# Performance work log

Measured on AMD Instinct MI355X. Metric: run time of the kernel, lower is better.

The kernel has to match this reference:

```python
import jax, jax.numpy as jnp
import numpy as np

N_NODES = 100000
N_EDGES = 1600000
D_IN = 128
D_OUT = 128


def setup_inputs() -> dict:
    key = jax.random.key(0)
    k_x, k_r, k_c, k_v, k_w = jax.random.split(key, 5)
    X = jax.random.normal(k_x, (N_NODES, D_IN), dtype=jnp.float32)
    A_rows = jax.random.randint(k_r, (N_EDGES,), 0, N_NODES, dtype=jnp.int32)
    A_cols = jax.random.randint(k_c, (N_EDGES,), 0, N_NODES, dtype=jnp.int32)
    A_vals = jax.random.uniform(k_v, (N_EDGES,), dtype=jnp.float32)
    # Xavier-uniform linear weight [out, in], zero bias (matches reset_parameters)
    limit = float(np.sqrt(6.0 / (D_IN + D_OUT)))
    W = jax.random.uniform(k_w, (D_OUT, D_IN), dtype=jnp.float32, minval=-limit, maxval=limit)
    b = jnp.zeros((D_OUT,), dtype=jnp.float32)
    return {"X": X, "A_rows": A_rows, "A_cols": A_cols, "A_vals": A_vals, "W": W, "b": b}


def reference(X, A_rows, A_cols, A_vals, W, b):
    # h = A_sparse @ X  (COO SpMM: gather neighbor features, scale, scatter-add by row)
    msgs = A_vals[:, None] * X[A_cols]          # [E, D_IN]
    h = jax.ops.segment_sum(msgs, A_rows, num_segments=N_NODES)  # [N, D_IN]
    # dense linear projection
    return h @ W.T + b
```

## Files before the change

kernel.cpp:

```cpp
#include <hip/hip_runtime.h>

#define N_NODES_C 100000
#define N_EDGES_C 1600000
#define D_C 128
#define NBKT 1563
#define RPB 64
#define CAP 1536
#define PTILE 4096
#define NPB ((N_EDGES_C + PTILE - 1) / PTILE)
#define NGB ((N_NODES_C + 63) / 64)
#define WB_STRIDE 136

static __device__ __forceinline__ unsigned short f2bf(float x) {
    unsigned u = __float_as_uint(x);
    unsigned r = 0x7fffu + ((u >> 16) & 1u);
    return (unsigned short)((u + r) >> 16);
}
static __device__ __forceinline__ float bflo(unsigned u) { return __uint_as_float(u << 16); }
static __device__ __forceinline__ float bfhi(unsigned u) { return __uint_as_float(u & 0xffff0000u); }

typedef __attribute__((ext_vector_type(8))) __bf16 bf16x8;
typedef __attribute__((ext_vector_type(4))) float f32x4;
union FragU { uint4 u; bf16x8 b; };

__global__ __launch_bounds__(256) void prep(const float* __restrict__ W,
                                            unsigned short* __restrict__ Wbf,
                                            int* __restrict__ gcount) {
    int t = blockIdx.x * 256 + threadIdx.x;
    if (t < 4096) {
        float4 w = ((const float4*)W)[t];
        uint2 p;
        p.x = (unsigned)f2bf(w.x) | ((unsigned)f2bf(w.y) << 16);
        p.y = (unsigned)f2bf(w.z) | ((unsigned)f2bf(w.w) << 16);
        ((uint2*)Wbf)[t] = p;
    } else {
        int j = t - 4096;
        if (j < NBKT) gcount[j] = 0;
    }
}

union SMemF {
    struct {
        int lhist[NBKT];
        int lbase[NBKT];
        unsigned short ebkt[PTILE];
        unsigned short ernk[PTILE];
    } part;
    unsigned short wb[128 * WB_STRIDE];
};

__global__ __launch_bounds__(256) void fused(const float* __restrict__ X,
                                             const int* __restrict__ rows,
                                             const int* __restrict__ cols,
                                             const float* __restrict__ vals,
                                             const unsigned short* __restrict__ Wbf,
                                             int* __restrict__ gcount,
                                             int2* __restrict__ staging,
                                             unsigned short* __restrict__ Y,
                                             int n, int E) {
    __shared__ SMemF sm;
    const int tid = threadIdx.x;

    if (blockIdx.x < NPB) {
        const int t0 = blockIdx.x * PTILE;

        for (int i = tid; i < NBKT; i += 256) sm.part.lhist[i] = 0;
        __syncthreads();

#pragma unroll
        for (int k = 0; k < PTILE / 256; ++k) {
            int e = t0 + k * 256 + tid;
            if (e < E) {
                int bkt = rows[e] >> 6;
                int rnk = atomicAdd(&sm.part.lhist[bkt], 1);
                sm.part.ebkt[k * 256 + tid] = (unsigned short)bkt;
                sm.part.ernk[k * 256 + tid] = (unsigned short)rnk;
            }
        }
        __syncthreads();

        for (int i = tid; i < NBKT; i += 256)
            sm.part.lbase[i] = sm.part.lhist[i] ? atomicAdd(&gcount[i], sm.part.lhist[i]) : 0;
        __syncthreads();

#pragma unroll
        for (int k = 0; k < PTILE / 256; ++k) {
            int e = t0 + k * 256 + tid;
            if (e < E) {
                int li = k * 256 + tid;
                int bkt = sm.part.ebkt[li];
                int dst = sm.part.lbase[bkt] + sm.part.ernk[li];
                if (dst < CAP) {
                    int rl = rows[e] & (RPB - 1);
                    int2 p;
                    p.x = cols[e] | (rl << 17);
                    p.y = __float_as_int(vals[e]);
                    staging[(long)bkt * CAP + dst] = p;
                }
            }
        }
        return;
    }

    const int g = blockIdx.x - NPB;
    const int wave = tid >> 6;
    const int lane = tid & 63;
    const int m16 = lane & 15;
    const int quad = lane >> 4;

    for (int i = tid; i < 128 * 16; i += 256) {
        int o = i >> 4;
        int k8 = (i & 15) * 8;
        *(uint4*)&sm.wb[o * WB_STRIDE + k8] = *(const uint4*)&Wbf[o * D_C + k8];
    }

    const int row0 = g * 64 + wave * 16;
    int row = row0 + m16;
    int rowc = (row < n) ? row : (n - 1);

    FragU a[4];
    const float* xp = X + (long)rowc * D_C + quad * 8;
#pragma unroll
    for (int s = 0; s < 4; ++s) {
        float4 x0 = *(const float4*)(xp + s * 32);
        float4 x1 = *(const float4*)(xp + s * 32 + 4);
        a[s].u.x = (unsigned)f2bf(x0.x) | ((unsigned)f2bf(x0.y) << 16);
        a[s].u.y = (unsigned)f2bf(x0.z) | ((unsigned)f2bf(x0.w) << 16);
        a[s].u.z = (unsigned)f2bf(x1.x) | ((unsigned)f2bf(x1.y) << 16);
        a[s].u.w = (unsigned)f2bf(x1.z) | ((unsigned)f2bf(x1.w) << 16);
    }
    __syncthreads();

    f32x4 acc[8];
#pragma unroll
    for (int t = 0; t < 8; ++t) acc[t] = (f32x4){0.f, 0.f, 0.f, 0.f};

#pragma unroll
    for (int s = 0; s < 4; ++s) {
#pragma unroll
        for (int t = 0; t < 8; ++t) {
            FragU bf;
            bf.u = *(const uint4*)&sm.wb[(t * 16 + m16) * WB_STRIDE + s * 32 + quad * 8];
            acc[t] = __builtin_amdgcn_mfma_f32_16x16x32_bf16(a[s].b, bf.b, acc[t], 0, 0, 0);
        }
    }

    __syncthreads();
    unsigned short* yt = sm.wb + wave * (16 * WB_STRIDE);
#pragma unroll
    for (int t = 0; t < 8; ++t)
#pragma unroll
        for (int r = 0; r < 4; ++r)
            yt[(quad * 4 + r) * WB_STRIDE + t * 16 + m16] = f2bf(acc[t][r]);
    __syncthreads();

#pragma unroll
    for (int h = 0; h < 2; ++h) {
        int row_l = h * 8 + (lane >> 3);
        int orow = row0 + row_l;
        if (orow < n) {
            const unsigned short* src = &yt[row_l * WB_STRIDE + (lane & 7) * 16];
            uint4 v0 = *(const uint4*)(src);
            uint4 v1 = *(const uint4*)(src + 8);
            uint4* dst = (uint4*)&Y[(long)orow * D_C + (lane & 7) * 16];
            dst[0] = v0;
            dst[1] = v1;
        }
    }
}

__global__ __launch_bounds__(256) void sort_aggregate(const int* __restrict__ gcount,
                                                      const int2* __restrict__ staging,
                                                      const unsigned short* __restrict__ Y,
                                                      const float* __restrict__ bias,
                                                      float* __restrict__ out, int n) {
    __shared__ int2 pl[CAP];
    __shared__ int hist[RPB];
    __shared__ int lcur[RPB];
    __shared__ int rbegL[RPB];
    __shared__ int rcntL[RPB];

    const int bb = blockIdx.x, tid = threadIdx.x;
    int cnt = gcount[bb];
    if (cnt > CAP) cnt = CAP;
    const long s = (long)bb * CAP;

    if (tid < RPB) hist[tid] = 0;
    __syncthreads();

    for (int i = tid; i < cnt; i += 256) {
        int rl = ((unsigned)staging[s + i].x) >> 17;
        atomicAdd(&hist[rl], 1);
    }
    __syncthreads();

    int v = (tid < RPB) ? hist[tid] : 0;
    for (int off = 1; off < RPB; off <<= 1) {
        int t = (tid >= off && tid < RPB) ? hist[tid - off] : 0;
        __syncthreads();
        if (tid < RPB) hist[tid] += t;
        __syncthreads();
    }
    if (tid < RPB) {
        int excl = hist[tid] - v;
        lcur[tid] = excl;
        rbegL[tid] = excl;
        rcntL[tid] = v;
    }
    __syncthreads();

    for (int i = tid; i < cnt; i += 256) {
        int2 p = staging[s + i];
        int rl = ((unsigned)p.x) >> 17;
        int slot = atomicAdd(&lcur[rl], 1);
        pl[slot] = p;
    }
    __syncthreads();

    const int lane = tid & 15;
    const unsigned short* Yl = Y + lane * 8;
    float4 b0 = *(const float4*)&bias[lane * 8];
    float4 b1 = *(const float4*)&bias[lane * 8 + 4];

#pragma unroll
    for (int pass = 0; pass < RPB / 16; ++pass) {
        int rlocal = pass * 16 + (tid >> 4);
        int row = bb * RPB + rlocal;
        if (row >= n) continue;

        int i = rbegL[rlocal];
        int e = i + rcntL[rlocal];

        float acc[8];
        acc[0] = b0.x; acc[1] = b0.y; acc[2] = b0.z; acc[3] = b0.w;
        acc[4] = b1.x; acc[5] = b1.y; acc[6] = b1.z; acc[7] = b1.w;

        for (; i + 8 <= e; i += 8) {
            int2 p[8];
            uint4 y[8];
#pragma unroll
            for (int u = 0; u < 8; ++u) p[u] = pl[i + u];
#pragma unroll
            for (int u = 0; u < 8; ++u)
                y[u] = *(const uint4*)&Yl[(long)(p[u].x & 0x1FFFF) * D_C];
#pragma unroll
            for (int u = 0; u < 8; ++u) {
                float v2 = __int_as_float(p[u].y);
                acc[0] += v2 * bflo(y[u].x); acc[1] += v2 * bfhi(y[u].x);
                acc[2] += v2 * bflo(y[u].y); acc[3] += v2 * bfhi(y[u].y);
                acc[4] += v2 * bflo(y[u].z); acc[5] += v2 * bfhi(y[u].z);
                acc[6] += v2 * bflo(y[u].w); acc[7] += v2 * bfhi(y[u].w);
            }
        }
        for (; i + 4 <= e; i += 4) {
            int2 p[4];
            uint4 y[4];
#pragma unroll
            for (int u = 0; u < 4; ++u) p[u] = pl[i + u];
#pragma unroll
            for (int u = 0; u < 4; ++u)
                y[u] = *(const uint4*)&Yl[(long)(p[u].x & 0x1FFFF) * D_C];
#pragma unroll
            for (int u = 0; u < 4; ++u) {
                float v2 = __int_as_float(p[u].y);
                acc[0] += v2 * bflo(y[u].x); acc[1] += v2 * bfhi(y[u].x);
                acc[2] += v2 * bflo(y[u].y); acc[3] += v2 * bfhi(y[u].y);
                acc[4] += v2 * bflo(y[u].z); acc[5] += v2 * bfhi(y[u].z);
                acc[6] += v2 * bflo(y[u].w); acc[7] += v2 * bfhi(y[u].w);
            }
        }
        for (; i < e; ++i) {
            int2 p = pl[i];
            uint4 y = *(const uint4*)&Yl[(long)(p.x & 0x1FFFF) * D_C];
            float v2 = __int_as_float(p.y);
            acc[0] += v2 * bflo(y.x); acc[1] += v2 * bfhi(y.x);
            acc[2] += v2 * bflo(y.y); acc[3] += v2 * bfhi(y.y);
            acc[4] += v2 * bflo(y.z); acc[5] += v2 * bfhi(y.z);
            acc[6] += v2 * bflo(y.w); acc[7] += v2 * bfhi(y.w);
        }

        f32x4 o0 = {acc[0], acc[1], acc[2], acc[3]};
        f32x4 o1 = {acc[4], acc[5], acc[6], acc[7]};
        f32x4* op = (f32x4*)&out[(long)row * D_C + lane * 8];
        __builtin_nontemporal_store(o0, op);
        __builtin_nontemporal_store(o1, op + 1);
    }
}

__global__ __launch_bounds__(256) void gemm_mfma(const float* __restrict__ X,
                                                 const float* __restrict__ W,
                                                 unsigned short* __restrict__ Y, int n) {
    __shared__ unsigned short Wb[128 * WB_STRIDE];

    const int tid = threadIdx.x;
    const int wave = tid >> 6;
    const int lane = tid & 63;
    const int m16 = lane & 15;
    const int quad = lane >> 4;

    const int row0 = blockIdx.x * 64 + wave * 16;
    int row = row0 + m16;
    int rowc = (row < n) ? row : (n - 1);

    float4 xv[4][2];
    const float* xp = X + (long)rowc * D_C + quad * 8;
#pragma unroll
    for (int s = 0; s < 4; ++s) {
        xv[s][0] = *(const float4*)(xp + s * 32);
        xv[s][1] = *(const float4*)(xp + s * 32 + 4);
    }

    for (int i = tid; i < 128 * 32; i += 256) {
        int o = i >> 5;
        int k4 = (i & 31) * 4;
        float4 w = *(const float4*)&W[o * 128 + k4];
        uint2 p;
        p.x = (unsigned)f2bf(w.x) | ((unsigned)f2bf(w.y) << 16);
        p.y = (unsigned)f2bf(w.z) | ((unsigned)f2bf(w.w) << 16);
        *(uint2*)&Wb[o * WB_STRIDE + k4] = p;
    }
    __syncthreads();

    FragU a[4];
#pragma unroll
    for (int s = 0; s < 4; ++s) {
        a[s].u.x = (unsigned)f2bf(xv[s][0].x) | ((unsigned)f2bf(xv[s][0].y) << 16);
        a[s].u.y = (unsigned)f2bf(xv[s][0].z) | ((unsigned)f2bf(xv[s][0].w) << 16);
        a[s].u.z = (unsigned)f2bf(xv[s][1].x) | ((unsigned)f2bf(xv[s][1].y) << 16);
        a[s].u.w = (unsigned)f2bf(xv[s][1].z) | ((unsigned)f2bf(xv[s][1].w) << 16);
    }

    f32x4 acc[8];
#pragma unroll
    for (int t = 0; t < 8; ++t) acc[t] = (f32x4){0.f, 0.f, 0.f, 0.f};

#pragma unroll
    for (int s = 0; s < 4; ++s) {
#pragma unroll
        for (int t = 0; t < 8; ++t) {
            FragU bf;
            bf.u = *(const uint4*)&Wb[(t * 16 + m16) * WB_STRIDE + s * 32 + quad * 8];
            acc[t] = __builtin_amdgcn_mfma_f32_16x16x32_bf16(a[s].b, bf.b, acc[t], 0, 0, 0);
        }
    }

#pragma unroll
    for (int t = 0; t < 8; ++t) {
#pragma unroll
        for (int r = 0; r < 4; ++r) {
            int orow = row0 + quad * 4 + r;
            if (orow < n) Y[(long)orow * D_C + t * 16 + m16] = f2bf(acc[t][r]);
        }
    }
}

__global__ __launch_bounds__(256) void init_out(const float* __restrict__ b,
                                                float* __restrict__ out, int n) {
    int idx = blockIdx.x * 256 + threadIdx.x;
    int total = n * (D_C / 4);
    if (idx < total) {
        int o4 = idx & (D_C / 4 - 1);
        ((float4*)out)[idx] = ((const float4*)b)[o4];
    }
}

__global__ __launch_bounds__(256) void scatter_edges(const int* __restrict__ rows,
                                                     const int* __restrict__ cols,
                                                     const float* __restrict__ vals,
                                                     const unsigned short* __restrict__ Y,
                                                     float* __restrict__ out, int E) {
    int e = blockIdx.x * 8 + (threadIdx.x >> 5);
    if (e >= E) return;
    int lane = threadIdx.x & 31;
    int row = rows[e];
    int col = cols[e];
    float v = vals[e];
    uint2 y = *(const uint2*)&Y[(long)col * D_C + lane * 4];
    float* dst = out + (long)row * D_C + lane * 4;
    unsafeAtomicAdd(dst + 0, v * bflo(y.x));
    unsafeAtomicAdd(dst + 1, v * bfhi(y.x));
    unsafeAtomicAdd(dst + 2, v * bflo(y.y));
    unsafeAtomicAdd(dst + 3, v * bfhi(y.y));
}

extern "C" void kernel_launch(void* const* d_in, const int* in_sizes, int n_in,
                              void* d_out, int out_size, void* d_ws, size_t ws_size,
                              hipStream_t stream) {
    const float* X  = (const float*)d_in[0];
    const int*   Ar = (const int*)d_in[1];
    const int*   Ac = (const int*)d_in[2];
    const float* Av = (const float*)d_in[3];
    const float* W  = (const float*)d_in[4];
    const float* b  = (const float*)d_in[5];
    float* out = (float*)d_out;

    unsigned short* Y = (unsigned short*)d_ws;
    int2* staging = (int2*)(Y + 12800000);
    unsigned short* Wbf = (unsigned short*)(staging + (size_t)NBKT * CAP);
    int* gcount = (int*)(Wbf + 16384);
    size_t need = (size_t)12800000 * 2 + (size_t)NBKT * CAP * 8 + 32768 + (size_t)NBKT * 4;

    if (ws_size >= need) {
        prep<<<23, 256, 0, stream>>>(W, Wbf, gcount);
        fused<<<NPB + NGB, 256, 0, stream>>>(X, Ar, Ac, Av, Wbf, gcount, staging, Y,
                                             N_NODES_C, N_EDGES_C);
        sort_aggregate<<<NBKT, 256, 0, stream>>>(gcount, staging, Y, b, out, N_NODES_C);
    } else {
        gemm_mfma<<<(N_NODES_C + 63) / 64, 256, 0, stream>>>(X, W, Y, N_NODES_C);
        init_out<<<(N_NODES_C * (D_C / 4) + 255) / 256, 256, 0, stream>>>(b, out, N_NODES_C);
        scatter_edges<<<(N_EDGES_C + 7) / 8, 256, 0, stream>>>(Ar, Ac, Av, Y, out, N_EDGES_C);
    }
}
```

Measured before the change: 226.1 us.

## Write GEMM output in permuted column layout directly from MFMA registers

The fused GEMM stage now packs MFMA accumulators straight into a permuted column order in Y, skipping the shared-memory transpose and its two barriers. The aggregate stage un-permutes at store time with strided per-element nontemporal stores and uses a bias vector permuted in prep. Staging entries are also held in registers so the sort reads them from global memory once instead of twice. The scattered 4-byte output stores are less coalesced than the old 16-byte vector stores, which may cost write bandwidth.

```diff
diff --git a/kernel.cpp b/kernel.cpp
--- a/kernel.cpp
+++ b/kernel.cpp
@@ -24,8 +24,10 @@
 union FragU { uint4 u; bf16x8 b; };
 
 __global__ __launch_bounds__(256) void prep(const float* __restrict__ W,
+                                            const float* __restrict__ b,
                                             unsigned short* __restrict__ Wbf,
-                                            int* __restrict__ gcount) {
+                                            int* __restrict__ gcount,
+                                            float* __restrict__ pbias) {
     int t = blockIdx.x * 256 + threadIdx.x;
     if (t < 4096) {
         float4 w = ((const float4*)W)[t];
@@ -33,9 +35,11 @@
         p.x = (unsigned)f2bf(w.x) | ((unsigned)f2bf(w.y) << 16);
         p.y = (unsigned)f2bf(w.z) | ((unsigned)f2bf(w.w) << 16);
         ((uint2*)Wbf)[t] = p;
+    } else if (t < 4096 + NBKT) {
+        gcount[t - 4096] = 0;
     } else {
-        int j = t - 4096;
-        if (j < NBKT) gcount[j] = 0;
+        int k = t - (4096 + NBKT);
+        if (k < 128) pbias[k] = b[(k & 7) * 16 + (k >> 3)];
     }
 }
 
@@ -145,26 +149,16 @@
         }
     }
 
-    __syncthreads();
-    unsigned short* yt = sm.wb + wave * (16 * WB_STRIDE);
-#pragma unroll
-    for (int t = 0; t < 8; ++t)
-#pragma unroll
-        for (int r = 0; r < 4; ++r)
-            yt[(quad * 4 + r) * WB_STRIDE + t * 16 + m16] = f2bf(acc[t][r]);
-    __syncthreads();
-
-#pragma unroll
-    for (int h = 0; h < 2; ++h) {
-        int row_l = h * 8 + (lane >> 3);
-        int orow = row0 + row_l;
+#pragma unroll
+    for (int r = 0; r < 4; ++r) {
+        int orow = row0 + quad * 4 + r;
         if (orow < n) {
-            const unsigned short* src = &yt[row_l * WB_STRIDE + (lane & 7) * 16];
-            uint4 v0 = *(const uint4*)(src);
-            uint4 v1 = *(const uint4*)(src + 8);
-            uint4* dst = (uint4*)&Y[(long)orow * D_C + (lane & 7) * 16];
-            dst[0] = v0;
-            dst[1] = v1;
+            uint4 v;
+            v.x = (unsigned)f2bf(acc[0][r]) | ((unsigned)f2bf(acc[1][r]) << 16);
+            v.y = (unsigned)f2bf(acc[2][r]) | ((unsigned)f2bf(acc[3][r]) << 16);
+            v.z = (unsigned)f2bf(acc[4][r]) | ((unsigned)f2bf(acc[5][r]) << 16);
+            v.w = (unsigned)f2bf(acc[6][r]) | ((unsigned)f2bf(acc[7][r]) << 16);
+            *(uint4*)&Y[(long)orow * D_C + m16 * 8] = v;
         }
     }
 }
@@ -172,7 +166,7 @@
 __global__ __launch_bounds__(256) void sort_aggregate(const int* __restrict__ gcount,
                                                       const int2* __restrict__ staging,
                                                       const unsigned short* __restrict__ Y,
-                                                      const float* __restrict__ bias,
+                                                      const float* __restrict__ pbias,
                                                       float* __restrict__ out, int n) {
     __shared__ int2 pl[CAP];
     __shared__ int hist[RPB];
@@ -188,9 +182,16 @@
     if (tid < RPB) hist[tid] = 0;
     __syncthreads();
 
-    for (int i = tid; i < cnt; i += 256) {
-        int rl = ((unsigned)staging[s + i].x) >> 17;
-        atomicAdd(&hist[rl], 1);
+    int2 p_reg[6];
+#pragma unroll
+    for (int k = 0; k < 6; ++k) {
+        int i = k * 256 + tid;
+        if (i < cnt) p_reg[k] = staging[s + i];
+    }
+#pragma unroll
+    for (int k = 0; k < 6; ++k) {
+        int i = k * 256 + tid;
+        if (i < cnt) atomicAdd(&hist[((unsigned)p_reg[k].x) >> 17], 1);
     }
     __syncthreads();
 
@@ -209,18 +210,21 @@
     }
     __syncthreads();
 
-    for (int i = tid; i < cnt; i += 256) {
-        int2 p = staging[s + i];
-        int rl = ((unsigned)p.x) >> 17;
-        int slot = atomicAdd(&lcur[rl], 1);
-        pl[slot] = p;
+#pragma unroll
+    for (int k = 0; k < 6; ++k) {
+        int i = k * 256 + tid;
+        if (i < cnt) {
+            int rl = ((unsigned)p_reg[k].x) >> 17;
+            int slot = atomicAdd(&lcur[rl], 1);
+            pl[slot] = p_reg[k];
+        }
     }
     __syncthreads();
 
     const int lane = tid & 15;
     const unsigned short* Yl = Y + lane * 8;
-    float4 b0 = *(const float4*)&bias[lane * 8];
-    float4 b1 = *(const float4*)&bias[lane * 8 + 4];
+    float4 b0 = *(const float4*)&pbias[lane * 8];
+    float4 b1 = *(const float4*)&pbias[lane * 8 + 4];
 
 #pragma unroll
     for (int pass = 0; pass < RPB / 16; ++pass) {
@@ -279,11 +283,10 @@
             acc[6] += v2 * bflo(y.w); acc[7] += v2 * bfhi(y.w);
         }
 
-        f32x4 o0 = {acc[0], acc[1], acc[2], acc[3]};
-        f32x4 o1 = {acc[4], acc[5], acc[6], acc[7]};
-        f32x4* op = (f32x4*)&out[(long)row * D_C + lane * 8];
-        __builtin_nontemporal_store(o0, op);
-        __builtin_nontemporal_store(o1, op + 1);
+        float* op = out + (long)row * D_C + lane;
+#pragma unroll
+        for (int j = 0; j < 8; ++j)
+            __builtin_nontemporal_store(acc[j], op + j * 16);
     }
 }
 
@@ -398,13 +401,15 @@
     int2* staging = (int2*)(Y + 12800000);
     unsigned short* Wbf = (unsigned short*)(staging + (size_t)NBKT * CAP);
     int* gcount = (int*)(Wbf + 16384);
-    size_t need = (size_t)12800000 * 2 + (size_t)NBKT * CAP * 8 + 32768 + (size_t)NBKT * 4;
+    float* pbias = (float*)(gcount + NBKT);
+    size_t need = (size_t)12800000 * 2 + (size_t)NBKT * CAP * 8 + 32768 +
+                  (size_t)NBKT * 4 + 512;
 
     if (ws_size >= need) {
-        prep<<<23, 256, 0, stream>>>(W, Wbf, gcount);
+        prep<<<23, 256, 0, stream>>>(W, b, Wbf, gcount, pbias);
         fused<<<NPB + NGB, 256, 0, stream>>>(X, Ar, Ac, Av, Wbf, gcount, staging, Y,
                                              N_NODES_C, N_EDGES_C);
-        sort_aggregate<<<NBKT, 256, 0, stream>>>(gcount, staging, Y, b, out, N_NODES_C);
+        sort_aggregate<<<NBKT, 256, 0, stream>>>(gcount, staging, Y, pbias, out, N_NODES_C);
     } else {
         gemm_mfma<<<(N_NODES_C + 63) / 64, 256, 0, stream>>>(X, W, Y, N_NODES_C);
         init_out<<<(N_NODES_C * (D_C / 4) + 255) / 256, 256, 0, stream>>>(b, out, N_NODES_C);
```

New measurement: 219.4 us. -2.9%, faster.
